# Optimization experiments

Hardware: AMD Instinct MI355X
Metric: run time of the kernel (lower is better)

The kernel has to match this reference:

```python
import jax, jax.numpy as jnp
import numpy as np


def _gcn_conv(x, edge_index_sl, deg_inv_sqrt, W, b, num_nodes):
    """One GCNConv layer (PyG semantics, normalize=True, self-loops already in edge_index_sl)."""
    h = x @ W  # [N, F_out] dense projection first (F_out <= F_in)
    src = edge_index_sl[0]
    dst = edge_index_sl[1]
    norm = deg_inv_sqrt[src] * deg_inv_sqrt[dst]  # [E+N]
    msg = h[src] * norm[:, None]                  # gather + scale
    out = jax.ops.segment_sum(msg, dst, num_segments=num_nodes)  # scatter-add
    return out + b


def _prep_graph(edge_index, num_nodes):
    # GCNConv(normalize=True) adds self-loops, then deg over destination nodes.
    loops = jnp.arange(num_nodes, dtype=edge_index.dtype)
    ei = jnp.concatenate([edge_index, jnp.stack([loops, loops])], axis=1)  # [2, E+N]
    deg = jax.ops.segment_sum(jnp.ones(ei.shape[1], dtype=jnp.float32), ei[1], num_segments=num_nodes)
    deg_inv_sqrt = jnp.where(deg > 0, jax.lax.rsqrt(deg), 0.0)
    return ei, deg_inv_sqrt


def setup_inputs() -> dict:
    key = jax.random.key(0)
    k1, k2, k3, k4 = jax.random.split(key, 4)
    N, E, D_IN, D_H, D_OUT = 100000, 1200000, 128, 64, 1
    x = jax.random.normal(k1, (N, D_IN), dtype=jnp.float32)
    edge_index = jax.random.randint(k2, (2, E), 0, N, dtype=jnp.int64)
    # Glorot-ish init for weights
    W1 = jax.random.normal(k3, (D_IN, D_H), dtype=jnp.float32) * (1.0 / np.sqrt(D_IN))
    b1 = jnp.zeros((D_H,), dtype=jnp.float32)
    W2 = jax.random.normal(k4, (D_H, D_OUT), dtype=jnp.float32) * (1.0 / np.sqrt(D_H))
    b2 = jnp.zeros((D_OUT,), dtype=jnp.float32)
    return {"x": x, "edge_index": edge_index, "W1": W1, "b1": b1, "W2": W2, "b2": b2}


def reference(x, edge_index, W1, b1, W2, b2):
    num_nodes = x.shape[0]
    ei, dinv = _prep_graph(edge_index, num_nodes)
    h = jax.nn.relu(_gcn_conv(x, ei, dinv, W1, b1, num_nodes))
    # F.dropout(training=self.training) is identity in eval mode (reference baseline)
    out = _gcn_conv(h, ei, dinv, W2, b2, num_nodes)
    return out
```

## Files before the change

### kernel.cpp

```cpp
#include <hip/hip_runtime.h>


#define NBLK 256
#define MAXB 8192

typedef __attribute__((ext_vector_type(8))) short bf16x8;
typedef __attribute__((ext_vector_type(4))) float f32x4;

__device__ __forceinline__ float bf2f(unsigned short u) {
    union { unsigned int i; float f; } v; v.i = ((unsigned int)u) << 16; return v.f;
}
__device__ __forceinline__ unsigned short f2bf(float f) {
    union { float f; unsigned int i; } v; v.f = f;
    unsigned int r = (v.i + 0x7fffu + ((v.i >> 16) & 1u)) >> 16;
    return (unsigned short)r;
}

__global__ __launch_bounds__(256) void k_packB(const float* __restrict__ W1,
                                               unsigned short* __restrict__ Bfrag) {
    for (int i = threadIdx.x; i < 8192; i += 256) {
        int j    = i & 7;
        int lane = (i >> 3) & 63;
        int ks   = (i >> 9) & 3;
        int nt   = i >> 11;
        int k = ks * 32 + ((lane >> 4) << 3) + j;
        int n = nt * 16 + (lane & 15);
        Bfrag[i] = f2bf(W1[k * 64 + n]);
    }
}

__global__ __launch_bounds__(256) void k_hist(const int* __restrict__ dst, int E, int chunk,
                                              int NB, int* __restrict__ bh) {
    __shared__ int h[512];
    int blk = blockIdx.x, t = threadIdx.x;
    h[t] = 0; h[t + 256] = 0;
    __syncthreads();
    int e0 = blk * chunk, e1 = min(E, e0 + chunk);
    for (int e = e0 + t; e < e1; e += 256) atomicAdd(&h[dst[e] >> 8], 1);
    __syncthreads();
    for (int k = t; k < NB; k += 256) bh[blk * NB + k] = h[k];
}

__global__ __launch_bounds__(256) void k_bscan(int* __restrict__ bh, int NB,
                                               int* __restrict__ btot) {
    __shared__ int s[256];
    int k = blockIdx.x, t = threadIdx.x;
    int v = bh[t * NB + k];
    s[t] = v;
    __syncthreads();
    for (int off = 1; off < 256; off <<= 1) {
        int u = (t >= off) ? s[t - off] : 0;
        __syncthreads();
        s[t] += u;
        __syncthreads();
    }
    bh[t * NB + k] = s[t] - v;
    if (t == 255) btot[k] = s[255];
}

__global__ __launch_bounds__(512) void k_cscan(const int* __restrict__ btot, int NB, int E,
                                               int* __restrict__ bbase, int* __restrict__ offs,
                                               int N) {
    __shared__ int s[512];
    int t = threadIdx.x;
    int v = (t < NB) ? btot[t] : 0;
    s[t] = v;
    __syncthreads();
    for (int off = 1; off < 512; off <<= 1) {
        int u = (t >= off) ? s[t - off] : 0;
        __syncthreads();
        s[t] += u;
        __syncthreads();
    }
    if (t < NB) bbase[t] = s[t] - v;
    if (t == 0) offs[N] = E;
}

__global__ __launch_bounds__(256) void k_dscatter(const int* __restrict__ src,
                                                  const int* __restrict__ dst, int E, int chunk,
                                                  const int* __restrict__ bh,
                                                  const int* __restrict__ bbase, int NB,
                                                  unsigned int* __restrict__ grouped) {
    __shared__ int cur[512];
    int blk = blockIdx.x, t = threadIdx.x;
    for (int k = t; k < NB; k += 256) cur[k] = bbase[k] + bh[blk * NB + k];
    __syncthreads();
    int e0 = blk * chunk, e1 = min(E, e0 + chunk);
    for (int e = e0 + t; e < e1; e += 256) {
        int d = dst[e];
        int pos = atomicAdd(&cur[d >> 8], 1);
        grouped[pos] = ((unsigned int)src[e] << 8) | (unsigned int)(d & 255);
    }
}

__global__ __launch_bounds__(256) void k_bfill(const unsigned int* __restrict__ grouped,
                                               const int* __restrict__ bbase,
                                               const int* __restrict__ btot, int N,
                                               int* __restrict__ offs, int* __restrict__ csr,
                                               float* __restrict__ dinv) {
    __shared__ int hist[256], pfx[256], cur[256];
    __shared__ int stage[MAXB];
    int k = blockIdx.x, t = threadIdx.x;
    int base = bbase[k], cnt = btot[k];
    hist[t] = 0;
    __syncthreads();
    for (int i = t; i < cnt; i += 256) atomicAdd(&hist[grouped[base + i] & 255u], 1);
    __syncthreads();
    int v = hist[t];
    pfx[t] = v;
    __syncthreads();
    for (int off = 1; off < 256; off <<= 1) {
        int u = (t >= off) ? pfx[t - off] : 0;
        __syncthreads();
        pfx[t] += u;
        __syncthreads();
    }
    int excl = pfx[t] - v;
    cur[t] = excl;
    int node = (k << 8) + t;
    if (node < N) {
        offs[node] = base + excl;
        dinv[node] = rsqrtf((float)v + 1.0f);
    }
    __syncthreads();
    if (cnt <= MAXB) {
        for (int i = t; i < cnt; i += 256) {
            unsigned int p = grouped[base + i];
            int pos = atomicAdd(&cur[p & 255u], 1);
            stage[pos] = (int)(p >> 8);
        }
        __syncthreads();
        for (int i = t; i < cnt; i += 256) csr[base + i] = stage[i];
    } else {
        for (int i = t; i < cnt; i += 256) {
            unsigned int p = grouped[base + i];
            int pos = atomicAdd(&cur[p & 255u], 1);
            csr[base + pos] = (int)(p >> 8);
        }
    }
}

__global__ __launch_bounds__(256) void k_gemm1m(
    const float* __restrict__ x, const unsigned short* __restrict__ Bfrag,
    const float* __restrict__ dinv, unsigned short* __restrict__ ppb, int N)
{
    int lane = threadIdx.x & 63;
    int wid = threadIdx.x >> 6;
    int r0 = blockIdx.x * 64 + wid * 16;
    int arow = r0 + (lane & 15);
    if (arow > N - 1) arow = N - 1;
    const float* xrow = x + (size_t)arow * 128 + ((lane >> 4) << 3);

    f32x4 acc0 = {0.f, 0.f, 0.f, 0.f};
    f32x4 acc1 = {0.f, 0.f, 0.f, 0.f};
    f32x4 acc2 = {0.f, 0.f, 0.f, 0.f};
    f32x4 acc3 = {0.f, 0.f, 0.f, 0.f};

    #pragma unroll
    for (int ks = 0; ks < 4; ks++) {
        float4 a0 = *(const float4*)(xrow + ks * 32);
        float4 a1 = *(const float4*)(xrow + ks * 32 + 4);
        bf16x8 a;
        a[0] = (short)f2bf(a0.x); a[1] = (short)f2bf(a0.y);
        a[2] = (short)f2bf(a0.z); a[3] = (short)f2bf(a0.w);
        a[4] = (short)f2bf(a1.x); a[5] = (short)f2bf(a1.y);
        a[6] = (short)f2bf(a1.z); a[7] = (short)f2bf(a1.w);
        const bf16x8* bp = (const bf16x8*)(Bfrag + (size_t)ks * 64 * 8 + lane * 8);
        acc0 = __builtin_amdgcn_mfma_f32_16x16x32_bf16(a, bp[0 * 256], acc0, 0, 0, 0);
        acc1 = __builtin_amdgcn_mfma_f32_16x16x32_bf16(a, bp[1 * 256], acc1, 0, 0, 0);
        acc2 = __builtin_amdgcn_mfma_f32_16x16x32_bf16(a, bp[2 * 256], acc2, 0, 0, 0);
        acc3 = __builtin_amdgcn_mfma_f32_16x16x32_bf16(a, bp[3 * 256], acc3, 0, 0, 0);
    }

    int c = lane & 15;
    int rbase = r0 + ((lane >> 4) << 2);
    #pragma unroll
    for (int j = 0; j < 4; j++) {
        int row = rbase + j;
        if (row < N) {
            float di = dinv[row];
            unsigned short* p = ppb + (size_t)row * 64 + c;
            p[0]  = f2bf(acc0[j] * di);
            p[16] = f2bf(acc1[j] * di);
            p[32] = f2bf(acc2[j] * di);
            p[48] = f2bf(acc3[j] * di);
        }
    }
}

__global__ void k_fused1(const int* __restrict__ offs, const int* __restrict__ csr,
                         const unsigned short* __restrict__ ppb,
                         const float* __restrict__ dinv, const float* __restrict__ b1,
                         const float* __restrict__ W2, float* __restrict__ qp, int N) {
    int t = blockIdx.x * blockDim.x + threadIdx.x;
    int lane = t & 63;
    int half = lane >> 5;
    int hl = lane & 31;
    int node = t >> 6;
    int nstride = (gridDim.x * blockDim.x) >> 6;
    float w2a = W2[2 * hl], w2b = W2[2 * hl + 1];
    float ba = b1[2 * hl], bb = b1[2 * hl + 1];
    for (; node < N; node += nstride) {
        int start = offs[node], end = offs[node + 1];
        float acca = 0.0f, accb = 0.0f;
        if (half == 0) {
            unsigned int v = *(const unsigned int*)&ppb[(size_t)node * 64 + 2 * hl];
            acca = bf2f((unsigned short)v);
            accb = bf2f((unsigned short)(v >> 16));
        }
        for (int j0 = start; j0 < end; j0 += 64) {
            int jj = j0 + lane;
            int idx = (jj < end) ? csr[jj] : 0;
            int m = end - j0; if (m > 64) m = 64;
            for (int kk = 0; kk < m; kk += 8) {
                int sidx[4]; bool act[4];
                #pragma unroll
                for (int q = 0; q < 4; q++) {
                    int ka = kk + 2 * q, kb = ka + 1;
                    int kac = (ka < m) ? ka : m - 1;
                    int kbc = (kb < m) ? kb : m - 1;
                    int s0 = __shfl(idx, kac, 64);
                    int s1 = __shfl(idx, kbc, 64);
                    sidx[q] = half ? s1 : s0;
                    act[q] = half ? (kb < m) : (ka < m);
                }
                unsigned int v[4];
                #pragma unroll
                for (int q = 0; q < 4; q++)
                    if (act[q]) v[q] = *(const unsigned int*)&ppb[(size_t)sidx[q] * 64 + 2 * hl];
                #pragma unroll
                for (int q = 0; q < 4; q++)
                    if (act[q]) {
                        acca += bf2f((unsigned short)(v[q] & 0xffffu));
                        accb += bf2f((unsigned short)(v[q] >> 16));
                    }
            }
        }
        acca += __shfl_xor(acca, 32, 64);
        accb += __shfl_xor(accb, 32, 64);
        float di = dinv[node];
        float ha = fmaxf(di * acca + ba, 0.0f);
        float hb = fmaxf(di * accb + bb, 0.0f);
        float v = ha * w2a + hb * w2b;
        #pragma unroll
        for (int mm = 16; mm > 0; mm >>= 1) v += __shfl_xor(v, mm, 64);
        if (lane == 0) qp[node] = v * di;
    }
}

__global__ void k_fused2(const int* __restrict__ offs, const int* __restrict__ csr,
                         const float* __restrict__ qp, const float* __restrict__ dinv,
                         const float* __restrict__ b2, float* __restrict__ out, int N) {
    int i = blockIdx.x * blockDim.x + threadIdx.x;
    if (i < N) {
        int start = offs[i], end = offs[i + 1];
        float s = qp[i];
        for (int j = start; j < end; j++) s += qp[csr[j]];
        out[i] = dinv[i] * s + b2[0];
    }
}

extern "C" void kernel_launch(void* const* d_in, const int* in_sizes, int n_in,
                              void* d_out, int out_size, void* d_ws, size_t ws_size,
                              hipStream_t stream) {
    const float* x  = (const float*)d_in[0];
    const int*   ei = (const int*)d_in[1];
    const float* W1 = (const float*)d_in[2];
    const float* b1 = (const float*)d_in[3];
    const float* W2 = (const float*)d_in[4];
    const float* b2 = (const float*)d_in[5];
    float* out = (float*)d_out;

    int N = in_sizes[0] / 128;
    int E = in_sizes[1] / 2;
    const int* src = ei;
    const int* dst = ei + E;
    int NB = (N + 255) >> 8;
    int chunk = (E + NBLK - 1) / NBLK;

    size_t Np = ((size_t)N + 255) & ~(size_t)255;
    size_t Ep = ((size_t)E + 255) & ~(size_t)255;
    char* w = (char*)d_ws;
    int* bh      = (int*)w;            w += (size_t)NBLK * 512 * 4;
    int* btot    = (int*)w;            w += 512 * 4;
    int* bbase   = (int*)w;            w += 512 * 4;
    unsigned int* grouped = (unsigned int*)w;  w += Ep * 4;
    int* offs    = (int*)w;            w += (Np + 256) * 4;
    int* csr     = (int*)w;            w += Ep * 4;
    float* dinv  = (float*)w;          w += Np * 4;
    unsigned short* ppb = (unsigned short*)w;  w += Np * 64 * 2;
    float* qp    = (float*)w;          w += Np * 4;
    unsigned short* Bfrag = (unsigned short*)w;

    k_packB<<<1, 256, 0, stream>>>(W1, Bfrag);
    k_hist<<<NBLK, 256, 0, stream>>>(dst, E, chunk, NB, bh);
    k_bscan<<<NB, 256, 0, stream>>>(bh, NB, btot);
    k_cscan<<<1, 512, 0, stream>>>(btot, NB, E, bbase, offs, N);
    k_dscatter<<<NBLK, 256, 0, stream>>>(src, dst, E, chunk, bh, bbase, NB, grouped);
    k_bfill<<<NB, 256, 0, stream>>>(grouped, bbase, btot, N, offs, csr, dinv);
    k_gemm1m<<<(N + 63) / 64, 256, 0, stream>>>(x, Bfrag, dinv, ppb, N);
    k_fused1<<<2048, 256, 0, stream>>>(offs, csr, ppb, dinv, b1, W2, qp, N);
    k_fused2<<<(N + 255) / 256, 256, 0, stream>>>(offs, csr, qp, dinv, b2, out, N);
}
```

Before: 197.5 us.

## Widen fused1 gather to 16-byte rows, merge packB into cscan, unroll fused2

```diff
diff --git a/kernel.cpp b/kernel.cpp
--- a/kernel.cpp
+++ b/kernel.cpp
@@ -16,9 +16,53 @@
     return (unsigned short)r;
 }
 
-__global__ __launch_bounds__(256) void k_packB(const float* __restrict__ W1,
+__global__ __launch_bounds__(256) void k_hist(const int* __restrict__ dst, int E, int chunk,
+                                              int NB, int* __restrict__ bh) {
+    __shared__ int h[512];
+    int blk = blockIdx.x, t = threadIdx.x;
+    h[t] = 0; h[t + 256] = 0;
+    __syncthreads();
+    int e0 = blk * chunk, e1 = min(E, e0 + chunk);
+    for (int e = e0 + t; e < e1; e += 256) atomicAdd(&h[dst[e] >> 8], 1);
+    __syncthreads();
+    for (int k = t; k < NB; k += 256) bh[blk * NB + k] = h[k];
+}
+
+__global__ __launch_bounds__(256) void k_bscan(int* __restrict__ bh, int NB,
+                                               int* __restrict__ btot) {
+    __shared__ int s[256];
+    int k = blockIdx.x, t = threadIdx.x;
+    int v = bh[t * NB + k];
+    s[t] = v;
+    __syncthreads();
+    for (int off = 1; off < 256; off <<= 1) {
+        int u = (t >= off) ? s[t - off] : 0;
+        __syncthreads();
+        s[t] += u;
+        __syncthreads();
+    }
+    bh[t * NB + k] = s[t] - v;
+    if (t == 255) btot[k] = s[255];
+}
+
+__global__ __launch_bounds__(512) void k_cscan(const int* __restrict__ btot, int NB, int E,
+                                               int* __restrict__ bbase, int* __restrict__ offs,
+                                               int N, const float* __restrict__ W1,
                                                unsigned short* __restrict__ Bfrag) {
-    for (int i = threadIdx.x; i < 8192; i += 256) {
+    __shared__ int s[512];
+    int t = threadIdx.x;
+    int v = (t < NB) ? btot[t] : 0;
+    s[t] = v;
+    __syncthreads();
+    for (int off = 1; off < 512; off <<= 1) {
+        int u = (t >= off) ? s[t - off] : 0;
+        __syncthreads();
+        s[t] += u;
+        __syncthreads();
+    }
+    if (t < NB) bbase[t] = s[t] - v;
+    if (t == 0) offs[N] = E;
+    for (int i = t; i < 8192; i += 512) {
         int j    = i & 7;
         int lane = (i >> 3) & 63;
         int ks   = (i >> 9) & 3;
@@ -27,53 +71,6 @@
         int n = nt * 16 + (lane & 15);
         Bfrag[i] = f2bf(W1[k * 64 + n]);
     }
-}
-
-__global__ __launch_bounds__(256) void k_hist(const int* __restrict__ dst, int E, int chunk,
-                                              int NB, int* __restrict__ bh) {
-    __shared__ int h[512];
-    int blk = blockIdx.x, t = threadIdx.x;
-    h[t] = 0; h[t + 256] = 0;
-    __syncthreads();
-    int e0 = blk * chunk, e1 = min(E, e0 + chunk);
-    for (int e = e0 + t; e < e1; e += 256) atomicAdd(&h[dst[e] >> 8], 1);
-    __syncthreads();
-    for (int k = t; k < NB; k += 256) bh[blk * NB + k] = h[k];
-}
-
-__global__ __launch_bounds__(256) void k_bscan(int* __restrict__ bh, int NB,
-                                               int* __restrict__ btot) {
-    __shared__ int s[256];
-    int k = blockIdx.x, t = threadIdx.x;
-    int v = bh[t * NB + k];
-    s[t] = v;
-    __syncthreads();
-    for (int off = 1; off < 256; off <<= 1) {
-        int u = (t >= off) ? s[t - off] : 0;
-        __syncthreads();
-        s[t] += u;
-        __syncthreads();
-    }
-    bh[t * NB + k] = s[t] - v;
-    if (t == 255) btot[k] = s[255];
-}
-
-__global__ __launch_bounds__(512) void k_cscan(const int* __restrict__ btot, int NB, int E,
-                                               int* __restrict__ bbase, int* __restrict__ offs,
-                                               int N) {
-    __shared__ int s[512];
-    int t = threadIdx.x;
-    int v = (t < NB) ? btot[t] : 0;
-    s[t] = v;
-    __syncthreads();
-    for (int off = 1; off < 512; off <<= 1) {
-        int u = (t >= off) ? s[t - off] : 0;
-        __syncthreads();
-        s[t] += u;
-        __syncthreads();
-    }
-    if (t < NB) bbase[t] = s[t] - v;
-    if (t == 0) offs[N] = E;
 }
 
 __global__ __launch_bounds__(256) void k_dscatter(const int* __restrict__ src,
@@ -194,56 +191,73 @@
                          const float* __restrict__ W2, float* __restrict__ qp, int N) {
     int t = blockIdx.x * blockDim.x + threadIdx.x;
     int lane = t & 63;
-    int half = lane >> 5;
-    int hl = lane & 31;
+    int eg = lane >> 3;
+    int c0 = (lane & 7) << 3;
     int node = t >> 6;
     int nstride = (gridDim.x * blockDim.x) >> 6;
-    float w2a = W2[2 * hl], w2b = W2[2 * hl + 1];
-    float ba = b1[2 * hl], bb = b1[2 * hl + 1];
+    float4 wA = *(const float4*)&W2[c0];
+    float4 wB = *(const float4*)&W2[c0 + 4];
+    float4 bA = *(const float4*)&b1[c0];
+    float4 bB = *(const float4*)&b1[c0 + 4];
     for (; node < N; node += nstride) {
         int start = offs[node], end = offs[node + 1];
-        float acca = 0.0f, accb = 0.0f;
-        if (half == 0) {
-            unsigned int v = *(const unsigned int*)&ppb[(size_t)node * 64 + 2 * hl];
-            acca = bf2f((unsigned short)v);
-            accb = bf2f((unsigned short)(v >> 16));
-        }
-        for (int j0 = start; j0 < end; j0 += 64) {
-            int jj = j0 + lane;
-            int idx = (jj < end) ? csr[jj] : 0;
-            int m = end - j0; if (m > 64) m = 64;
-            for (int kk = 0; kk < m; kk += 8) {
-                int sidx[4]; bool act[4];
-                #pragma unroll
-                for (int q = 0; q < 4; q++) {
-                    int ka = kk + 2 * q, kb = ka + 1;
-                    int kac = (ka < m) ? ka : m - 1;
-                    int kbc = (kb < m) ? kb : m - 1;
-                    int s0 = __shfl(idx, kac, 64);
-                    int s1 = __shfl(idx, kbc, 64);
-                    sidx[q] = half ? s1 : s0;
-                    act[q] = half ? (kb < m) : (ka < m);
+        float a0 = 0.f, a1 = 0.f, a2 = 0.f, a3 = 0.f;
+        float a4 = 0.f, a5 = 0.f, a6 = 0.f, a7 = 0.f;
+        if (eg == 0) {
+            uint4 v = *(const uint4*)&ppb[(size_t)node * 64 + c0];
+            a0 += bf2f((unsigned short)(v.x & 0xffffu));
+            a1 += bf2f((unsigned short)(v.x >> 16));
+            a2 += bf2f((unsigned short)(v.y & 0xffffu));
+            a3 += bf2f((unsigned short)(v.y >> 16));
+            a4 += bf2f((unsigned short)(v.z & 0xffffu));
+            a5 += bf2f((unsigned short)(v.z >> 16));
+            a6 += bf2f((unsigned short)(v.w & 0xffffu));
+            a7 += bf2f((unsigned short)(v.w >> 16));
+        }
+        for (int j0 = start; j0 < end; j0 += 32) {
+            bool act[4]; int idx[4];
+            #pragma unroll
+            for (int q = 0; q < 4; q++) {
+                int jj = j0 + 8 * q + eg;
+                act[q] = jj < end;
+                idx[q] = csr[act[q] ? jj : end - 1];
+            }
+            uint4 v[4];
+            #pragma unroll
+            for (int q = 0; q < 4; q++)
+                if (act[q]) v[q] = *(const uint4*)&ppb[(size_t)idx[q] * 64 + c0];
+            #pragma unroll
+            for (int q = 0; q < 4; q++)
+                if (act[q]) {
+                    a0 += bf2f((unsigned short)(v[q].x & 0xffffu));
+                    a1 += bf2f((unsigned short)(v[q].x >> 16));
+                    a2 += bf2f((unsigned short)(v[q].y & 0xffffu));
+                    a3 += bf2f((unsigned short)(v[q].y >> 16));
+                    a4 += bf2f((unsigned short)(v[q].z & 0xffffu));
+                    a5 += bf2f((unsigned short)(v[q].z >> 16));
+                    a6 += bf2f((unsigned short)(v[q].w & 0xffffu));
+                    a7 += bf2f((unsigned short)(v[q].w >> 16));
                 }
-                unsigned int v[4];
-                #pragma unroll
-                for (int q = 0; q < 4; q++)
-                    if (act[q]) v[q] = *(const unsigned int*)&ppb[(size_t)sidx[q] * 64 + 2 * hl];
-                #pragma unroll
-                for (int q = 0; q < 4; q++)
-                    if (act[q]) {
-                        acca += bf2f((unsigned short)(v[q] & 0xffffu));
-                        accb += bf2f((unsigned short)(v[q] >> 16));
-                    }
-            }
-        }
-        acca += __shfl_xor(acca, 32, 64);
-        accb += __shfl_xor(accb, 32, 64);
+        }
+        #pragma unroll
+        for (int m = 8; m <= 32; m <<= 1) {
+            a0 += __shfl_xor(a0, m, 64); a1 += __shfl_xor(a1, m, 64);
+            a2 += __shfl_xor(a2, m, 64); a3 += __shfl_xor(a3, m, 64);
+            a4 += __shfl_xor(a4, m, 64); a5 += __shfl_xor(a5, m, 64);
+            a6 += __shfl_xor(a6, m, 64); a7 += __shfl_xor(a7, m, 64);
+        }
         float di = dinv[node];
-        float ha = fmaxf(di * acca + ba, 0.0f);
-        float hb = fmaxf(di * accb + bb, 0.0f);
-        float v = ha * w2a + hb * w2b;
-        #pragma unroll
-        for (int mm = 16; mm > 0; mm >>= 1) v += __shfl_xor(v, mm, 64);
+        float v = fmaxf(di * a0 + bA.x, 0.f) * wA.x
+                + fmaxf(di * a1 + bA.y, 0.f) * wA.y
+                + fmaxf(di * a2 + bA.z, 0.f) * wA.z
+                + fmaxf(di * a3 + bA.w, 0.f) * wA.w
+                + fmaxf(di * a4 + bB.x, 0.f) * wB.x
+                + fmaxf(di * a5 + bB.y, 0.f) * wB.y
+                + fmaxf(di * a6 + bB.z, 0.f) * wB.z
+                + fmaxf(di * a7 + bB.w, 0.f) * wB.w;
+        v += __shfl_xor(v, 1, 64);
+        v += __shfl_xor(v, 2, 64);
+        v += __shfl_xor(v, 4, 64);
         if (lane == 0) qp[node] = v * di;
     }
 }
@@ -255,7 +269,13 @@
     if (i < N) {
         int start = offs[i], end = offs[i + 1];
         float s = qp[i];
-        for (int j = start; j < end; j++) s += qp[csr[j]];
+        int j = start;
+        for (; j + 4 <= end; j += 4) {
+            int c0 = csr[j], c1 = csr[j + 1], c2 = csr[j + 2], c3 = csr[j + 3];
+            float q0 = qp[c0], q1 = qp[c1], q2 = qp[c2], q3 = qp[c3];
+            s += (q0 + q1) + (q2 + q3);
+        }
+        for (; j < end; j++) s += qp[csr[j]];
         out[i] = dinv[i] * s + b2[0];
     }
 }
@@ -292,10 +312,9 @@
     float* qp    = (float*)w;          w += Np * 4;
     unsigned short* Bfrag = (unsigned short*)w;
 
-    k_packB<<<1, 256, 0, stream>>>(W1, Bfrag);
     k_hist<<<NBLK, 256, 0, stream>>>(dst, E, chunk, NB, bh);
     k_bscan<<<NB, 256, 0, stream>>>(bh, NB, btot);
-    k_cscan<<<1, 512, 0, stream>>>(btot, NB, E, bbase, offs, N);
+    k_cscan<<<1, 512, 0, stream>>>(btot, NB, E, bbase, offs, N, W1, Bfrag);
     k_dscatter<<<NBLK, 256, 0, stream>>>(src, dst, E, chunk, bh, bbase, NB, grouped);
     k_bfill<<<NB, 256, 0, stream>>>(grouped, bbase, btot, N, offs, csr, dinv);
     k_gemm1m<<<(N + 63) / 64, 256, 0, stream>>>(x, Bfrag, dinv, ppb, N);
```

Result: no change. 198.8 us (+0.6%).
